# Optimization experiments

Measured on AMD Instinct MI355X. Metric: run time of the kernel, lower is better.

The kernel has to match this reference:

```python
import jax, jax.numpy as jnp
import numpy as np

EPS = 1e-20
TEMP = 0.07
PATCH = 64
STEP = 32  # patch_size * overlap(0.5)


def zero_softmax(x, eps=1e-5):
    # ZeroSoftmax: ((exp(x)-1)^2) / (sum + eps), maps x==0 -> exactly 0 weight
    e = jnp.square(jnp.exp(x) - 1.0)
    return e / (jnp.sum(e, axis=-1, keepdims=True) + eps)


def _scaling_mask(H, W, p, step):
    # constant overlap-count mask from CRW.compute_scaling_mask (static shapes)
    sm = np.zeros((H, W), np.float32)
    for i in range(0, H - step, step):
        for j in range(0, W - step, step):
            sm[i:i + p, j:j + p] += 1.0
    return jnp.asarray(sm)


def _window_sums(m, p, step):
    # m: (B,T,SP,H,W) -> sliding-window sums (B,T,SP,nH,nW) via integral image
    ii = jnp.cumsum(jnp.cumsum(m, axis=-2), axis=-1)
    ii = jnp.pad(ii, ((0, 0), (0, 0), (0, 0), (1, 0), (1, 0)))
    H = m.shape[-2]
    nH = (H - p) // step + 1
    lo = jnp.arange(nH) * step
    hi = lo + p
    r_hi = ii[..., hi, :]   # (B,T,SP,nH,W+1)
    r_lo = ii[..., lo, :]
    return r_hi[..., hi] - r_hi[..., lo] - r_lo[..., hi] + r_lo[..., lo]


def setup_inputs() -> dict:
    key = jax.random.key(0)
    k1, k2, k3 = jax.random.split(key, 3)
    B, T, H, W = 2, 4, 256, 256
    nH = (H - PATCH) // STEP + 1  # 7
    N = nH * nH                   # 49 patches
    Cenc, D, SP = 512, 128, 64
    feats = jax.random.normal(k1, (B, N, Cenc, T), jnp.float32)
    W_head = jax.random.normal(k2, (Cenc, D), jnp.float32) / np.sqrt(Cenc)
    sp_mask = jax.random.randint(k3, (B, T, H, W), 0, SP, jnp.int32)
    return {"feats": feats, "W_head": W_head, "sp_mask": sp_mask, "max_sp_num": SP}


def reference(feats, W_head, sp_mask, max_sp_num):
    B, N, Cenc, T = feats.shape
    H, W = sp_mask.shape[-2:]
    SP = max_sp_num

    # --- pixels_to_nodes tail: projection head + L2 normalize over channel dim ---
    q = jnp.einsum('bnct,cd->bndt', feats, W_head)            # (B,N,128,T)
    nrm = jnp.maximum(jnp.linalg.norm(q, axis=2, keepdims=True), 1e-12)
    q = q / nrm
    q = jnp.transpose(q, (0, 2, 3, 1))                        # (B,128,T,N)

    # --- patches_to_sp_embeddings: windowed superpixel pooling ---
    oh = (sp_mask[:, :, None, :, :] ==
          jnp.arange(SP, dtype=sp_mask.dtype)[None, None, :, None, None]
          ).astype(jnp.float32)                               # (B,T,SP,H,W)
    sm = _scaling_mask(H, W, PATCH, STEP)                     # (H,W)
    ws = _window_sums(oh / sm, PATCH, STEP)                   # (B,T,SP,nH,nW)
    denom = jnp.sum(oh, axis=(-1, -2)) + EPS                  # (B,T,SP)
    wts = jnp.transpose(ws, (0, 1, 3, 4, 2)) / denom[:, :, None, None, :]
    wts = wts.reshape(B, T, N, SP)                            # (B,T,N,SP)
    q_sp = jnp.einsum('bdtn,btns->bdts', q, wts)              # (B,128,T,SP)

    # --- affinity + zero_softmax stochastic matrices ---
    As = jnp.einsum('bdtn,bdtm->btnm', q_sp[:, :, :-1], q_sp[:, :, 1:])  # (B,T-1,SP,SP)
    A12 = zero_softmax(As / TEMP)
    A21 = zero_softmax(jnp.swapaxes(As, -1, -2) / TEMP)

    # --- palindrome random walks + cross-entropy to cycle-consistency targets ---
    tgt = jnp.tile(jnp.arange(SP), B)
    loss = jnp.float32(0.0)
    AAs = []
    for i in range(1, T - 1):
        mats = [A12[:, k] for k in range(i + 1)] + [A21[:, k] for k in range(i, -1, -1)]
        aa = mats[0]
        for m in mats[1:]:
            aa = aa @ m
        AAs.append(aa)
        logits = jnp.log(aa + EPS).reshape(B * SP, SP)
        logp = jax.nn.log_softmax(logits, axis=-1)
        loss = loss + jnp.mean(-logp[jnp.arange(B * SP), tgt])
    return loss, jnp.stack(AAs)
```

## Files before the change

### kernel.cpp

```cpp
#include <hip/hip_runtime.h>
#include <hip/hip_bf16.h>

constexpr int NWIN = 49;
constexpr int QLD  = 52;

constexpr int OFF_WS   = 0;
constexpr int OFF_Q    = 26624;
constexpr int OFF_QSP  = 79872;
constexpr int OFF_A12  = 145408;
constexpr int OFF_A12T = 169984;
constexpr int OFF_A21  = 194560;
constexpr int OFF_A21T = 219136;

__global__ void __launch_bounds__(256, 1)
k_front(const int* __restrict__ mask, const float* __restrict__ feats,
        const float* __restrict__ Wh, float* __restrict__ ws, float* __restrict__ q) {
    if (blockIdx.x < 392) {
        int win = blockIdx.x % NWIN;
        int bt  = blockIdx.x / NWIN;
        int wy = win / 7, wx = win % 7;
        __shared__ float loc[64];
        if (threadIdx.x < 64) loc[threadIdx.x] = 0.f;
        __syncthreads();
        const int* base = mask + bt * 65536 + (wy * 32) * 256 + wx * 32;
        #pragma unroll
        for (int it = 0; it < 16; ++it) {
            int idx = it * 256 + (int)threadIdx.x;
            int r = idx >> 6, c = idx & 63;
            int s = base[r * 256 + c];
            int y = wy * 32 + r, x = wx * 32 + c;
            float w = 1.f;
            if (y >= 32 && y < 224) w *= 0.5f;
            if (x >= 32 && x < 224) w *= 0.5f;
            atomicAdd(&loc[s], w);
        }
        __syncthreads();
        if (threadIdx.x < 64) {
            ws[(bt * 64 + (int)threadIdx.x) * QLD + win] = loc[threadIdx.x];
        } else if (win == 0) {
            int s = threadIdx.x & 63;
            int col = 49 + (int)(threadIdx.x >> 6) - 1;
            ws[(bt * 64 + s) * QLD + col] = 0.f;
        }
    } else {
        int bid = blockIdx.x - 392;
        int n = bid % NWIN, b = bid / NWIN;
        __shared__ float4 f4[512];
        __shared__ float4 psum4[256];
        __shared__ float4 red4[2];
        const float4* fp4 = (const float4*)(feats + (size_t)(b * NWIN + n) * 2048);
        for (int i = threadIdx.x; i < 512; i += 256) f4[i] = fp4[i];
        __syncthreads();

        int d = threadIdx.x & 127, ch = threadIdx.x >> 7;
        float a0 = 0.f, a1 = 0.f, a2 = 0.f, a3 = 0.f;
        const float* wp = Wh + d;
        int c0 = ch * 256;
        #pragma unroll 8
        for (int c = c0; c < c0 + 256; ++c) {
            float w = wp[c * 128];
            float4 fv = f4[c];
            a0 += fv.x * w; a1 += fv.y * w; a2 += fv.z * w; a3 += fv.w * w;
        }
        psum4[threadIdx.x] = make_float4(a0, a1, a2, a3);
        __syncthreads();

        float4 A;
        if (threadIdx.x < 128) {
            float4 p0 = psum4[threadIdx.x], p1 = psum4[128 + threadIdx.x];
            A = make_float4(p0.x + p1.x, p0.y + p1.y, p0.z + p1.z, p0.w + p1.w);
            float sx = A.x * A.x, sy = A.y * A.y, sz = A.z * A.z, sw = A.w * A.w;
            for (int off = 32; off; off >>= 1) {
                sx += __shfl_down(sx, off); sy += __shfl_down(sy, off);
                sz += __shfl_down(sz, off); sw += __shfl_down(sw, off);
            }
            if ((threadIdx.x & 63) == 0) red4[threadIdx.x >> 6] = make_float4(sx, sy, sz, sw);
        }
        __syncthreads();
        if (threadIdx.x < 128) {
            float4 r0 = red4[0], r1 = red4[1];
            float ix = 1.f / fmaxf(sqrtf(r0.x + r1.x), 1e-12f);
            float iy = 1.f / fmaxf(sqrtf(r0.y + r1.y), 1e-12f);
            float iz = 1.f / fmaxf(sqrtf(r0.z + r1.z), 1e-12f);
            float iw = 1.f / fmaxf(sqrtf(r0.w + r1.w), 1e-12f);
            float* qb = q + (size_t)(b * 128 + d) * 4 * QLD + n;
            qb[0 * QLD] = A.x * ix;
            qb[1 * QLD] = A.y * iy;
            qb[2 * QLD] = A.z * iz;
            qb[3 * QLD] = A.w * iw;
        }
    }
}

__global__ void k_qsp(const float* __restrict__ q, const float* __restrict__ wsg,
                      float* __restrict__ qsp) {
    int tid = blockIdx.x * 256 + threadIdx.x;
    int s = tid & 63;
    int d = (tid >> 6) & 127;
    int t = (tid >> 13) & 3;
    int b = tid >> 15;
    const float4* qrow = (const float4*)(q + (size_t)((b * 128 + d) * 4 + t) * QLD);
    const float4* wrow = (const float4*)(wsg + (size_t)((b * 4 + t) * 64 + s) * QLD);
    float acc = 0.f, den = 0.f;
    #pragma unroll
    for (int i = 0; i < 13; ++i) {
        float4 w = wrow[i];
        float4 qv = qrow[i];
        den += w.x + w.y + w.z + w.w;
        acc += qv.x * w.x + qv.y * w.y + qv.z * w.z + qv.w * w.w;
    }
    qsp[tid] = acc / (den + 1e-20f);
}

__global__ void __launch_bounds__(256, 1)
k_as(const float* __restrict__ qsp,
     float* __restrict__ a12, float* __restrict__ a12T,
     float* __restrict__ a21, float* __restrict__ a21T, float* __restrict__ out) {
    int t = blockIdx.x % 3, b = blockIdx.x / 3;
    if (blockIdx.x == 0 && threadIdx.x == 0) out[0] = 0.f;
    __shared__ float4 qaT4[64 * 32];
    __shared__ float4 qbT4[64 * 32];
    const int tid = threadIdx.x;

    {
        const float4* gA = (const float4*)(qsp + (size_t)(b * 4 + t) * 8192);
        const float4* gB = (const float4*)(qsp + (size_t)(b * 4 + t + 1) * 8192);
        float* qaF = (float*)qaT4;
        float* qbF = (float*)qbT4;
        #pragma unroll
        for (int it = 0; it < 8; ++it) {
            int idx = it * 256 + tid;
            int d = idx >> 4, s0 = (idx & 15) << 2;
            float4 va = gA[idx];
            float4 vb = gB[idx];
            int g = d >> 2, c = d & 3;
            #pragma unroll
            for (int u = 0; u < 4; ++u) {
                int s = s0 + u;
                int w = (s * 32 + (g ^ (s & 31))) * 4 + c;
                float fa = (u == 0) ? va.x : (u == 1) ? va.y : (u == 2) ? va.z : va.w;
                float fb = (u == 0) ? vb.x : (u == 1) ? vb.y : (u == 2) ? vb.z : vb.w;
                qaF[w] = fa;
                qbF[w] = fb;
            }
        }
    }
    __syncthreads();

    const int nl = tid >> 4, ml = tid & 15;
    float acc[16];
    #pragma unroll
    for (int i = 0; i < 16; ++i) acc[i] = 0.f;
    #pragma unroll 8
    for (int k4 = 0; k4 < 32; ++k4) {
        float4 av[4], bv[4];
        #pragma unroll
        for (int i = 0; i < 4; ++i) { int n = nl + 16 * i; av[i] = qaT4[n * 32 + (k4 ^ (n & 31))]; }
        #pragma unroll
        for (int j = 0; j < 4; ++j) { int m = ml + 16 * j; bv[j] = qbT4[m * 32 + (k4 ^ (m & 31))]; }
        #pragma unroll
        for (int i = 0; i < 4; ++i)
            #pragma unroll
            for (int j = 0; j < 4; ++j)
                acc[i * 4 + j] += av[i].x * bv[j].x + av[i].y * bv[j].y
                                + av[i].z * bv[j].z + av[i].w * bv[j].w;
    }
    __syncthreads();

    float* eb = (float*)qaT4;
    float* rs = (float*)qbT4;
    float* cs = rs + 64;
    #pragma unroll
    for (int i = 0; i < 4; ++i)
        #pragma unroll
        for (int j = 0; j < 4; ++j) {
            int n = nl + 16 * i, m = ml + 16 * j;
            float x = acc[i * 4 + j] * (1.f / 0.07f);
            float e = expf(x) - 1.f;
            eb[n * 65 + m] = e * e;
        }
    __syncthreads();
    if (tid < 128) {
        int r = tid & 63; bool isrow = tid < 64;
        float a = 0.f;
        #pragma unroll
        for (int k = 0; k < 64; ++k) a += isrow ? eb[r * 65 + k] : eb[k * 65 + r];
        (isrow ? rs : cs)[r] = a + 1e-5f;
    }
    __syncthreads();
    float* p12  = a12  + (b * 3 + t) * 4096;
    float* p12T = a12T + (b * 3 + t) * 4096;
    float* p21  = a21  + (b * 3 + t) * 4096;
    float* p21T = a21T + (b * 3 + t) * 4096;
    #pragma unroll
    for (int i = 0; i < 4; ++i)
        #pragma unroll
        for (int j = 0; j < 4; ++j) {
            int n = nl + 16 * i, m = ml + 16 * j;
            float v   = eb[n * 65 + m];
            float v12 = v / rs[n];
            float v21 = v / cs[m];
            p12 [n * 64 + m] = v12;
            p12T[m * 64 + n] = v12;
            p21 [m * 64 + n] = v21;
            p21T[n * 64 + m] = v21;
        }
}


__device__ __forceinline__ void dump_mat(float* M, const float4* v) {
    #pragma unroll
    for (int it = 0; it < 4; ++it) {
        int idx = it * 256 + (int)threadIdx.x;
        int r = idx >> 4, c4 = (idx & 15) << 2;
        *(float4*)&M[r * 64 + (c4 ^ ((r & 15) << 2))] = v[it];
    }
}

__device__ __forceinline__ void mmh_sw(float* acc, const float* Ra, const float* Rb) {
    int lt = threadIdx.x & 127;
    int nl = lt >> 3, ml = lt & 7;
    int sxa = nl << 2;
    #pragma unroll
    for (int k0 = 0; k0 < 64; k0 += 4) {
        float4 av[4], bv[8];
        #pragma unroll
        for (int i = 0; i < 4; ++i)
            av[i] = *(const float4*)&Ra[(nl + 16 * i) * 64 + (k0 ^ sxa)];
        #pragma unroll
        for (int j = 0; j < 8; ++j) {
            int m = ml + 8 * j;
            bv[j] = *(const float4*)&Rb[m * 64 + (k0 ^ ((m & 15) << 2))];
        }
        #pragma unroll
        for (int i = 0; i < 4; ++i)
            #pragma unroll
            for (int j = 0; j < 8; ++j)
                acc[i * 8 + j] += av[i].x * bv[j].x + av[i].y * bv[j].y
                                + av[i].z * bv[j].z + av[i].w * bv[j].w;
    }
}

__device__ __forceinline__ void wrh_sw(float* M, const float* acc) {
    int lt = threadIdx.x & 127;
    int nl = lt >> 3, ml = lt & 7;
    #pragma unroll
    for (int i = 0; i < 4; ++i)
        #pragma unroll
        for (int j = 0; j < 8; ++j) {
            int r = nl + 16 * i, k = ml + 8 * j;
            M[r * 64 + (((k & ~3) ^ ((r & 15) << 2)) | (k & 3))] = acc[i * 8 + j];
        }
}

__device__ __forceinline__ void mm256_sw(float* acc, const float* Ra, const float* Rb) {
    int tid = threadIdx.x;
    int nl = tid >> 4, ml = tid & 15;
    int sxa = nl << 2, sxb = ml << 2;
    #pragma unroll
    for (int i = 0; i < 16; ++i) acc[i] = 0.f;
    #pragma unroll 4
    for (int k0 = 0; k0 < 64; k0 += 4) {
        float4 av[4], bv[4];
        #pragma unroll
        for (int i = 0; i < 4; ++i)
            av[i] = *(const float4*)&Ra[(nl + 16 * i) * 64 + (k0 ^ sxa)];
        #pragma unroll
        for (int j = 0; j < 4; ++j)
            bv[j] = *(const float4*)&Rb[(ml + 16 * j) * 64 + (k0 ^ sxb)];
        #pragma unroll
        for (int i = 0; i < 4; ++i)
            #pragma unroll
            for (int j = 0; j < 4; ++j)
                acc[i * 4 + j] += av[i].x * bv[j].x + av[i].y * bv[j].y
                                + av[i].z * bv[j].z + av[i].w * bv[j].w;
    }
}

__device__ __forceinline__ void store_loss(const float* acc, float* __restrict__ aa,
                                           float* __restrict__ out, float* red) {
    int tid = threadIdx.x;
    int nl = tid >> 4, ml = tid & 15;
    #pragma unroll
    for (int i = 0; i < 4; ++i)
        #pragma unroll
        for (int j = 0; j < 4; ++j)
            aa[(nl + 16 * i) * 64 + (ml + 16 * j)] = acc[i * 4 + j];
    int l = tid & 63;
    float part = 0.f;
    #pragma unroll
    for (int i = 0; i < 4; ++i) {
        float rsum = acc[i * 4 + 0] + acc[i * 4 + 1] + acc[i * 4 + 2] + acc[i * 4 + 3];
        rsum += __shfl_down(rsum, 8, 16);
        rsum += __shfl_down(rsum, 4, 16);
        rsum += __shfl_down(rsum, 2, 16);
        rsum += __shfl_down(rsum, 1, 16);
        float dv = __shfl(acc[5 * i], (l & 48) | nl, 64);
        if ((l & 15) == 0) part += logf(rsum + 6.4e-19f) - logf(dv + 1e-20f);
    }
    for (int off = 32; off; off >>= 1) part += __shfl_down(part, off);
    if (l == 0) red[tid >> 6] = part;
    __syncthreads();
    if (tid == 0) atomicAdd(out, (red[0] + red[1] + red[2] + red[3]) * (1.f / 128.f));
}

__global__ void __launch_bounds__(256, 1)
k_chain(const float* __restrict__ a12, const float* __restrict__ a12T,
        const float* __restrict__ a21, const float* __restrict__ a21T,
        float* __restrict__ out) {
    int path = blockIdx.x & 1, b = blockIdx.x >> 1;
    __shared__ float M[4 * 4096];
    float* M0 = M;
    float* M1 = M + 4096;
    float* M2 = M + 8192;
    float* M3 = M + 12288;
    const int tid = threadIdx.x;

    const float4* L0 = (const float4*)(a12  + (b * 3 + 0) * 4096);
    const float4* L1 = (const float4*)(a12T + (b * 3 + 1) * 4096);
    const float4* L2 = (const float4*)(a21T + (b * 3 + 0) * 4096);
    const float4* L3 = (const float4*)(a21  + (b * 3 + 1) * 4096);
    const float4* L4 = (const float4*)(a12T + (b * 3 + 2) * 4096);
    const float4* L5 = (const float4*)(a21  + (b * 3 + 2) * 4096);

    float4 pf[6][4];
    #pragma unroll
    for (int it = 0; it < 4; ++it) {
        int idx = it * 256 + tid;
        pf[0][it] = L0[idx];
        pf[1][it] = L1[idx];
        pf[2][it] = L2[idx];
        pf[3][it] = L3[idx];
    }
    if (path) {
        #pragma unroll
        for (int it = 0; it < 4; ++it) {
            int idx = it * 256 + tid;
            pf[4][it] = L4[idx];
            pf[5][it] = L5[idx];
        }
    }
    dump_mat(M0, pf[0]);
    dump_mat(M1, pf[1]);
    dump_mat(M2, pf[2]);
    dump_mat(M3, pf[3]);
    __syncthreads();

    int half = tid >> 7;
    float hacc[32];
    #pragma unroll
    for (int i = 0; i < 32; ++i) hacc[i] = 0.f;
    mmh_sw(hacc, half ? M2 : M0, half ? M3 : M1);
    __syncthreads();
    wrh_sw(half ? M3 : M1, hacc);
    if (path) { dump_mat(M0, pf[4]); dump_mat(M2, pf[5]); }
    __syncthreads();

    if (path == 0) {
        float acc[16];
        mm256_sw(acc, M1, M3);
        store_loss(acc, out + 1 + b * 4096, out, M0);
    } else {
        float hacc2[32];
        #pragma unroll
        for (int i = 0; i < 32; ++i) hacc2[i] = 0.f;
        mmh_sw(hacc2, half ? M3 : M1, half ? M2 : M0);
        __syncthreads();
        wrh_sw(half ? M1 : M0, hacc2);
        __syncthreads();
        float acc[16];
        mm256_sw(acc, M0, M1);
        store_loss(acc, out + 1 + (2 + b) * 4096, out, M2);
    }
}

extern "C" void kernel_launch(void* const* d_in, const int* in_sizes, int n_in,
                              void* d_out, int out_size, void* d_ws, size_t ws_size,
                              hipStream_t stream) {
    const float* feats = (const float*)d_in[0];
    const float* Wh    = (const float*)d_in[1];
    const int*   mask  = (const int*)d_in[2];
    float* out = (float*)d_out;
    float* ws  = (float*)d_ws;

    float* ws_sums = ws + OFF_WS;
    float* q       = ws + OFF_Q;
    float* qsp     = ws + OFF_QSP;
    float* a12     = ws + OFF_A12;
    float* a12T    = ws + OFF_A12T;
    float* a21     = ws + OFF_A21;
    float* a21T    = ws + OFF_A21T;

    k_front<<<392 + 2 * NWIN, 256, 0, stream>>>(mask, feats, Wh, ws_sums, q);
    k_qsp<<<256, 256, 0, stream>>>(q, ws_sums, qsp);
    k_as<<<6, 256, 0, stream>>>(qsp, a12, a12T, a21, a21T, out);
    k_chain<<<4, 256, 0, stream>>>(a12, a12T, a21, a21T, out);
}
```

Before: 118.3 us.

## Fuse four kernels into one persistent kernel with global atomic barriers

Merges the front, qsp, affinity and chain kernels into a single 256-block kernel that steps through the stages, separated by software grid barriers built on atomic counters. Front work units are spread over the 256 blocks, some of which handle two units. The goal is to remove three kernel launch gaps and their tail latency. In exchange it adds a memset launch, spin-wait barriers that rely on all 256 blocks being resident at once, and serialised front work on some blocks.

```diff
diff --git a/kernel.cpp b/kernel.cpp
--- a/kernel.cpp
+++ b/kernel.cpp
@@ -11,15 +11,29 @@
 constexpr int OFF_A12T = 169984;
 constexpr int OFF_A21  = 194560;
 constexpr int OFF_A21T = 219136;
-
-__global__ void __launch_bounds__(256, 1)
-k_front(const int* __restrict__ mask, const float* __restrict__ feats,
-        const float* __restrict__ Wh, float* __restrict__ ws, float* __restrict__ q) {
-    if (blockIdx.x < 392) {
-        int win = blockIdx.x % NWIN;
-        int bt  = blockIdx.x / NWIN;
+constexpr int OFF_BAR  = 243712;
+
+__device__ __forceinline__ void gbar(int* c) {
+    __syncthreads();
+    if (threadIdx.x == 0) {
+        __threadfence();
+        atomicAdd(c, 1);
+        while (atomicAdd(c, 0) < 256) __builtin_amdgcn_s_sleep(2);
+        __threadfence();
+    }
+    __syncthreads();
+}
+
+__device__ __forceinline__ void front_unit(int u, const int* __restrict__ mask,
+                                           const float* __restrict__ feats,
+                                           const float* __restrict__ Wh,
+                                           float* __restrict__ ws,
+                                           float* __restrict__ q, float* SMEM) {
+    if (u < 392) {
+        int win = u % NWIN;
+        int bt  = u / NWIN;
         int wy = win / 7, wx = win % 7;
-        __shared__ float loc[64];
+        float* loc = SMEM;
         if (threadIdx.x < 64) loc[threadIdx.x] = 0.f;
         __syncthreads();
         const int* base = mask + bt * 65536 + (wy * 32) * 256 + wx * 32;
@@ -43,11 +57,11 @@
             ws[(bt * 64 + s) * QLD + col] = 0.f;
         }
     } else {
-        int bid = blockIdx.x - 392;
+        int bid = u - 392;
         int n = bid % NWIN, b = bid / NWIN;
-        __shared__ float4 f4[512];
-        __shared__ float4 psum4[256];
-        __shared__ float4 red4[2];
+        float4* f4    = (float4*)(SMEM + 64);
+        float4* psum4 = f4 + 512;
+        float4* red4  = psum4 + 256;
         const float4* fp4 = (const float4*)(feats + (size_t)(b * NWIN + n) * 2048);
         for (int i = threadIdx.x; i < 512; i += 256) f4[i] = fp4[i];
         __syncthreads();
@@ -92,122 +106,6 @@
     }
 }
 
-__global__ void k_qsp(const float* __restrict__ q, const float* __restrict__ wsg,
-                      float* __restrict__ qsp) {
-    int tid = blockIdx.x * 256 + threadIdx.x;
-    int s = tid & 63;
-    int d = (tid >> 6) & 127;
-    int t = (tid >> 13) & 3;
-    int b = tid >> 15;
-    const float4* qrow = (const float4*)(q + (size_t)((b * 128 + d) * 4 + t) * QLD);
-    const float4* wrow = (const float4*)(wsg + (size_t)((b * 4 + t) * 64 + s) * QLD);
-    float acc = 0.f, den = 0.f;
-    #pragma unroll
-    for (int i = 0; i < 13; ++i) {
-        float4 w = wrow[i];
-        float4 qv = qrow[i];
-        den += w.x + w.y + w.z + w.w;
-        acc += qv.x * w.x + qv.y * w.y + qv.z * w.z + qv.w * w.w;
-    }
-    qsp[tid] = acc / (den + 1e-20f);
-}
-
-__global__ void __launch_bounds__(256, 1)
-k_as(const float* __restrict__ qsp,
-     float* __restrict__ a12, float* __restrict__ a12T,
-     float* __restrict__ a21, float* __restrict__ a21T, float* __restrict__ out) {
-    int t = blockIdx.x % 3, b = blockIdx.x / 3;
-    if (blockIdx.x == 0 && threadIdx.x == 0) out[0] = 0.f;
-    __shared__ float4 qaT4[64 * 32];
-    __shared__ float4 qbT4[64 * 32];
-    const int tid = threadIdx.x;
-
-    {
-        const float4* gA = (const float4*)(qsp + (size_t)(b * 4 + t) * 8192);
-        const float4* gB = (const float4*)(qsp + (size_t)(b * 4 + t + 1) * 8192);
-        float* qaF = (float*)qaT4;
-        float* qbF = (float*)qbT4;
-        #pragma unroll
-        for (int it = 0; it < 8; ++it) {
-            int idx = it * 256 + tid;
-            int d = idx >> 4, s0 = (idx & 15) << 2;
-            float4 va = gA[idx];
-            float4 vb = gB[idx];
-            int g = d >> 2, c = d & 3;
-            #pragma unroll
-            for (int u = 0; u < 4; ++u) {
-                int s = s0 + u;
-                int w = (s * 32 + (g ^ (s & 31))) * 4 + c;
-                float fa = (u == 0) ? va.x : (u == 1) ? va.y : (u == 2) ? va.z : va.w;
-                float fb = (u == 0) ? vb.x : (u == 1) ? vb.y : (u == 2) ? vb.z : vb.w;
-                qaF[w] = fa;
-                qbF[w] = fb;
-            }
-        }
-    }
-    __syncthreads();
-
-    const int nl = tid >> 4, ml = tid & 15;
-    float acc[16];
-    #pragma unroll
-    for (int i = 0; i < 16; ++i) acc[i] = 0.f;
-    #pragma unroll 8
-    for (int k4 = 0; k4 < 32; ++k4) {
-        float4 av[4], bv[4];
-        #pragma unroll
-        for (int i = 0; i < 4; ++i) { int n = nl + 16 * i; av[i] = qaT4[n * 32 + (k4 ^ (n & 31))]; }
-        #pragma unroll
-        for (int j = 0; j < 4; ++j) { int m = ml + 16 * j; bv[j] = qbT4[m * 32 + (k4 ^ (m & 31))]; }
-        #pragma unroll
-        for (int i = 0; i < 4; ++i)
-            #pragma unroll
-            for (int j = 0; j < 4; ++j)
-                acc[i * 4 + j] += av[i].x * bv[j].x + av[i].y * bv[j].y
-                                + av[i].z * bv[j].z + av[i].w * bv[j].w;
-    }
-    __syncthreads();
-
-    float* eb = (float*)qaT4;
-    float* rs = (float*)qbT4;
-    float* cs = rs + 64;
-    #pragma unroll
-    for (int i = 0; i < 4; ++i)
-        #pragma unroll
-        for (int j = 0; j < 4; ++j) {
-            int n = nl + 16 * i, m = ml + 16 * j;
-            float x = acc[i * 4 + j] * (1.f / 0.07f);
-            float e = expf(x) - 1.f;
-            eb[n * 65 + m] = e * e;
-        }
-    __syncthreads();
-    if (tid < 128) {
-        int r = tid & 63; bool isrow = tid < 64;
-        float a = 0.f;
-        #pragma unroll
-        for (int k = 0; k < 64; ++k) a += isrow ? eb[r * 65 + k] : eb[k * 65 + r];
-        (isrow ? rs : cs)[r] = a + 1e-5f;
-    }
-    __syncthreads();
-    float* p12  = a12  + (b * 3 + t) * 4096;
-    float* p12T = a12T + (b * 3 + t) * 4096;
-    float* p21  = a21  + (b * 3 + t) * 4096;
-    float* p21T = a21T + (b * 3 + t) * 4096;
-    #pragma unroll
-    for (int i = 0; i < 4; ++i)
-        #pragma unroll
-        for (int j = 0; j < 4; ++j) {
-            int n = nl + 16 * i, m = ml + 16 * j;
-            float v   = eb[n * 65 + m];
-            float v12 = v / rs[n];
-            float v21 = v / cs[m];
-            p12 [n * 64 + m] = v12;
-            p12T[m * 64 + n] = v12;
-            p21 [m * 64 + n] = v21;
-            p21T[n * 64 + m] = v21;
-        }
-}
-
-
 __device__ __forceinline__ void dump_mat(float* M, const float4* v) {
     #pragma unroll
     for (int it = 0; it < 4; ++it) {
@@ -305,72 +203,199 @@
 }
 
 __global__ void __launch_bounds__(256, 1)
-k_chain(const float* __restrict__ a12, const float* __restrict__ a12T,
-        const float* __restrict__ a21, const float* __restrict__ a21T,
-        float* __restrict__ out) {
-    int path = blockIdx.x & 1, b = blockIdx.x >> 1;
-    __shared__ float M[4 * 4096];
-    float* M0 = M;
-    float* M1 = M + 4096;
-    float* M2 = M + 8192;
-    float* M3 = M + 12288;
+k_all(const int* __restrict__ mask, const float* __restrict__ feats,
+      const float* __restrict__ Wh, float* __restrict__ ws,
+      float* __restrict__ q, float* __restrict__ qsp,
+      float* __restrict__ a12, float* __restrict__ a12T,
+      float* __restrict__ a21, float* __restrict__ a21T,
+      float* __restrict__ out, int* __restrict__ bars) {
+    __shared__ __align__(16) float SMEM[16384];
+    const int blk = blockIdx.x;
     const int tid = threadIdx.x;
 
-    const float4* L0 = (const float4*)(a12  + (b * 3 + 0) * 4096);
-    const float4* L1 = (const float4*)(a12T + (b * 3 + 1) * 4096);
-    const float4* L2 = (const float4*)(a21T + (b * 3 + 0) * 4096);
-    const float4* L3 = (const float4*)(a21  + (b * 3 + 1) * 4096);
-    const float4* L4 = (const float4*)(a12T + (b * 3 + 2) * 4096);
-    const float4* L5 = (const float4*)(a21  + (b * 3 + 2) * 4096);
-
-    float4 pf[6][4];
-    #pragma unroll
-    for (int it = 0; it < 4; ++it) {
-        int idx = it * 256 + tid;
-        pf[0][it] = L0[idx];
-        pf[1][it] = L1[idx];
-        pf[2][it] = L2[idx];
-        pf[3][it] = L3[idx];
-    }
-    if (path) {
+    front_unit(blk, mask, feats, Wh, ws, q, SMEM);
+    if (blk < 234) {
+        __syncthreads();
+        front_unit(blk + 256, mask, feats, Wh, ws, q, SMEM);
+    }
+    gbar(&bars[0]);
+
+    {
+        int t2 = blk * 256 + tid;
+        int s = t2 & 63;
+        int d = (t2 >> 6) & 127;
+        int t = (t2 >> 13) & 3;
+        int b = t2 >> 15;
+        const float4* qrow = (const float4*)(q + (size_t)((b * 128 + d) * 4 + t) * QLD);
+        const float4* wrow = (const float4*)(ws + (size_t)((b * 4 + t) * 64 + s) * QLD);
+        float acc = 0.f, den = 0.f;
+        #pragma unroll
+        for (int i = 0; i < 13; ++i) {
+            float4 w = wrow[i];
+            float4 qv = qrow[i];
+            den += w.x + w.y + w.z + w.w;
+            acc += qv.x * w.x + qv.y * w.y + qv.z * w.z + qv.w * w.w;
+        }
+        qsp[t2] = acc / (den + 1e-20f);
+    }
+    gbar(&bars[1]);
+
+    if (blk < 6) {
+        int t = blk % 3, b = blk / 3;
+        if (blk == 0 && tid == 0) out[0] = 0.f;
+        float4* qaT4 = (float4*)SMEM;
+        float4* qbT4 = qaT4 + 2048;
+
+        {
+            const float4* gA = (const float4*)(qsp + (size_t)(b * 4 + t) * 8192);
+            const float4* gB = (const float4*)(qsp + (size_t)(b * 4 + t + 1) * 8192);
+            float* qaF = (float*)qaT4;
+            float* qbF = (float*)qbT4;
+            #pragma unroll
+            for (int it = 0; it < 8; ++it) {
+                int idx = it * 256 + tid;
+                int d = idx >> 4, s0 = (idx & 15) << 2;
+                float4 va = gA[idx];
+                float4 vb = gB[idx];
+                int g = d >> 2, c = d & 3;
+                #pragma unroll
+                for (int u = 0; u < 4; ++u) {
+                    int s = s0 + u;
+                    int w = (s * 32 + (g ^ (s & 31))) * 4 + c;
+                    float fa = (u == 0) ? va.x : (u == 1) ? va.y : (u == 2) ? va.z : va.w;
+                    float fb = (u == 0) ? vb.x : (u == 1) ? vb.y : (u == 2) ? vb.z : vb.w;
+                    qaF[w] = fa;
+                    qbF[w] = fb;
+                }
+            }
+        }
+        __syncthreads();
+
+        const int nl = tid >> 4, ml = tid & 15;
+        float acc[16];
+        #pragma unroll
+        for (int i = 0; i < 16; ++i) acc[i] = 0.f;
+        #pragma unroll 8
+        for (int k4 = 0; k4 < 32; ++k4) {
+            float4 av[4], bv[4];
+            #pragma unroll
+            for (int i = 0; i < 4; ++i) { int n = nl + 16 * i; av[i] = qaT4[n * 32 + (k4 ^ (n & 31))]; }
+            #pragma unroll
+            for (int j = 0; j < 4; ++j) { int m = ml + 16 * j; bv[j] = qbT4[m * 32 + (k4 ^ (m & 31))]; }
+            #pragma unroll
+            for (int i = 0; i < 4; ++i)
+                #pragma unroll
+                for (int j = 0; j < 4; ++j)
+                    acc[i * 4 + j] += av[i].x * bv[j].x + av[i].y * bv[j].y
+                                    + av[i].z * bv[j].z + av[i].w * bv[j].w;
+        }
+        __syncthreads();
+
+        float* eb = (float*)qaT4;
+        float* rs = (float*)qbT4;
+        float* cs = rs + 64;
+        #pragma unroll
+        for (int i = 0; i < 4; ++i)
+            #pragma unroll
+            for (int j = 0; j < 4; ++j) {
+                int n = nl + 16 * i, m = ml + 16 * j;
+                float x = acc[i * 4 + j] * (1.f / 0.07f);
+                float e = expf(x) - 1.f;
+                eb[n * 65 + m] = e * e;
+            }
+        __syncthreads();
+        if (tid < 128) {
+            int r = tid & 63; bool isrow = tid < 64;
+            float a = 0.f;
+            #pragma unroll
+            for (int k = 0; k < 64; ++k) a += isrow ? eb[r * 65 + k] : eb[k * 65 + r];
+            (isrow ? rs : cs)[r] = a + 1e-5f;
+        }
+        __syncthreads();
+        float* p12  = a12  + (b * 3 + t) * 4096;
+        float* p12T = a12T + (b * 3 + t) * 4096;
+        float* p21  = a21  + (b * 3 + t) * 4096;
+        float* p21T = a21T + (b * 3 + t) * 4096;
+        #pragma unroll
+        for (int i = 0; i < 4; ++i)
+            #pragma unroll
+            for (int j = 0; j < 4; ++j) {
+                int n = nl + 16 * i, m = ml + 16 * j;
+                float v   = eb[n * 65 + m];
+                float v12 = v / rs[n];
+                float v21 = v / cs[m];
+                p12 [n * 64 + m] = v12;
+                p12T[m * 64 + n] = v12;
+                p21 [m * 64 + n] = v21;
+                p21T[n * 64 + m] = v21;
+            }
+    }
+    gbar(&bars[2]);
+
+    if (blk < 4) {
+        int path = blk & 1, b = blk >> 1;
+        float* M0 = SMEM;
+        float* M1 = SMEM + 4096;
+        float* M2 = SMEM + 8192;
+        float* M3 = SMEM + 12288;
+
+        const float4* L0 = (const float4*)(a12  + (b * 3 + 0) * 4096);
+        const float4* L1 = (const float4*)(a12T + (b * 3 + 1) * 4096);
+        const float4* L2 = (const float4*)(a21T + (b * 3 + 0) * 4096);
+        const float4* L3 = (const float4*)(a21  + (b * 3 + 1) * 4096);
+        const float4* L4 = (const float4*)(a12T + (b * 3 + 2) * 4096);
+        const float4* L5 = (const float4*)(a21  + (b * 3 + 2) * 4096);
+
+        float4 pf[6][4];
         #pragma unroll
         for (int it = 0; it < 4; ++it) {
             int idx = it * 256 + tid;
-            pf[4][it] = L4[idx];
-            pf[5][it] = L5[idx];
-        }
-    }
-    dump_mat(M0, pf[0]);
-    dump_mat(M1, pf[1]);
-    dump_mat(M2, pf[2]);
-    dump_mat(M3, pf[3]);
-    __syncthreads();
-
-    int half = tid >> 7;
-    float hacc[32];
-    #pragma unroll
-    for (int i = 0; i < 32; ++i) hacc[i] = 0.f;
-    mmh_sw(hacc, half ? M2 : M0, half ? M3 : M1);
-    __syncthreads();
-    wrh_sw(half ? M3 : M1, hacc);
-    if (path) { dump_mat(M0, pf[4]); dump_mat(M2, pf[5]); }
-    __syncthreads();
-
-    if (path == 0) {
-        float acc[16];
-        mm256_sw(acc, M1, M3);
-        store_loss(acc, out + 1 + b * 4096, out, M0);
-    } else {
-        float hacc2[32];
-        #pragma unroll
-        for (int i = 0; i < 32; ++i) hacc2[i] = 0.f;
-        mmh_sw(hacc2, half ? M3 : M1, half ? M2 : M0);
-        __syncthreads();
-        wrh_sw(half ? M1 : M0, hacc2);
-        __syncthreads();
-        float acc[16];
-        mm256_sw(acc, M0, M1);
-        store_loss(acc, out + 1 + (2 + b) * 4096, out, M2);
+            pf[0][it] = L0[idx];
+            pf[1][it] = L1[idx];
+            pf[2][it] = L2[idx];
+            pf[3][it] = L3[idx];
+        }
+        if (path) {
+            #pragma unroll
+            for (int it = 0; it < 4; ++it) {
+                int idx = it * 256 + tid;
+                pf[4][it] = L4[idx];
+                pf[5][it] = L5[idx];
+            }
+        }
+        __syncthreads();
+        dump_mat(M0, pf[0]);
+        dump_mat(M1, pf[1]);
+        dump_mat(M2, pf[2]);
+        dump_mat(M3, pf[3]);
+        __syncthreads();
+
+        int half = tid >> 7;
+        float hacc[32];
+        #pragma unroll
+        for (int i = 0; i < 32; ++i) hacc[i] = 0.f;
+        mmh_sw(hacc, half ? M2 : M0, half ? M3 : M1);
+        __syncthreads();
+        wrh_sw(half ? M3 : M1, hacc);
+        if (path) { dump_mat(M0, pf[4]); dump_mat(M2, pf[5]); }
+        __syncthreads();
+
+        if (path == 0) {
+            float acc[16];
+            mm256_sw(acc, M1, M3);
+            store_loss(acc, out + 1 + b * 4096, out, M0);
+        } else {
+            float hacc2[32];
+            #pragma unroll
+            for (int i = 0; i < 32; ++i) hacc2[i] = 0.f;
+            mmh_sw(hacc2, half ? M3 : M1, half ? M2 : M0);
+            __syncthreads();
+            wrh_sw(half ? M1 : M0, hacc2);
+            __syncthreads();
+            float acc[16];
+            mm256_sw(acc, M0, M1);
+            store_loss(acc, out + 1 + (2 + b) * 4096, out, M2);
+        }
     }
 }
 
@@ -390,9 +415,9 @@
     float* a12T    = ws + OFF_A12T;
     float* a21     = ws + OFF_A21;
     float* a21T    = ws + OFF_A21T;
-
-    k_front<<<392 + 2 * NWIN, 256, 0, stream>>>(mask, feats, Wh, ws_sums, q);
-    k_qsp<<<256, 256, 0, stream>>>(q, ws_sums, qsp);
-    k_as<<<6, 256, 0, stream>>>(qsp, a12, a12T, a21, a21T, out);
-    k_chain<<<4, 256, 0, stream>>>(a12, a12T, a21, a21T, out);
-}
+    int*   bars    = (int*)(ws + OFF_BAR);
+
+    hipMemsetAsync(bars, 0, 16, stream);
+    k_all<<<256, 256, 0, stream>>>(mask, feats, Wh, ws_sums, q, qsp,
+                                   a12, a12T, a21, a21T, out, bars);
+}
```

New measurement: 170.5 us. 44.1% more time.

## Fuse qsp, affinity and chain kernels into one with a global spin barrier

Applied to the files above, without the earlier changes.

Merges the superpixel pooling (qsp), the affinity/zero-softmax step and the random-walk chain into a single 6-block kernel. Each block recomputes its own two qsp slices in shared memory, in 32-channel chunks, rather than reading them from a separate kernel's global output. An atomic counter plus spin-wait with agent-scope fences replaces the kernel boundary between the affinity and chain stages. This removes two launches and the qsp round trip through global memory. In exchange the pooling work runs on only 6 blocks instead of 256, and correctness depends on all 6 blocks being co-resident for the spin barrier.

```diff
diff --git a/kernel.cpp b/kernel.cpp
--- a/kernel.cpp
+++ b/kernel.cpp
@@ -5,16 +5,25 @@
 constexpr int QLD  = 52;
 
 constexpr int OFF_WS   = 0;
-constexpr int OFF_Q    = 26624;
-constexpr int OFF_QSP  = 79872;
-constexpr int OFF_A12  = 145408;
-constexpr int OFF_A12T = 169984;
-constexpr int OFF_A21  = 194560;
-constexpr int OFF_A21T = 219136;
+constexpr int OFF_BAR  = 26624;
+constexpr int OFF_Q    = 26640;
+constexpr int OFF_A12  = 79888;
+constexpr int OFF_A12T = 104464;
+constexpr int OFF_A21  = 129040;
+constexpr int OFF_A21T = 153616;
+
+__device__ __forceinline__ void fence_rel() {
+    __builtin_amdgcn_fence(__ATOMIC_RELEASE, "agent");
+}
+__device__ __forceinline__ void fence_acq() {
+    __builtin_amdgcn_fence(__ATOMIC_ACQUIRE, "agent");
+}
 
 __global__ void __launch_bounds__(256, 1)
 k_front(const int* __restrict__ mask, const float* __restrict__ feats,
-        const float* __restrict__ Wh, float* __restrict__ ws, float* __restrict__ q) {
+        const float* __restrict__ Wh, float* __restrict__ ws, float* __restrict__ q,
+        int* __restrict__ bars) {
+    if (blockIdx.x == 0 && threadIdx.x == 0) bars[0] = 0;
     if (blockIdx.x < 392) {
         int win = blockIdx.x % NWIN;
         int bt  = blockIdx.x / NWIN;
@@ -92,122 +101,6 @@
     }
 }
 
-__global__ void k_qsp(const float* __restrict__ q, const float* __restrict__ wsg,
-                      float* __restrict__ qsp) {
-    int tid = blockIdx.x * 256 + threadIdx.x;
-    int s = tid & 63;
-    int d = (tid >> 6) & 127;
-    int t = (tid >> 13) & 3;
-    int b = tid >> 15;
-    const float4* qrow = (const float4*)(q + (size_t)((b * 128 + d) * 4 + t) * QLD);
-    const float4* wrow = (const float4*)(wsg + (size_t)((b * 4 + t) * 64 + s) * QLD);
-    float acc = 0.f, den = 0.f;
-    #pragma unroll
-    for (int i = 0; i < 13; ++i) {
-        float4 w = wrow[i];
-        float4 qv = qrow[i];
-        den += w.x + w.y + w.z + w.w;
-        acc += qv.x * w.x + qv.y * w.y + qv.z * w.z + qv.w * w.w;
-    }
-    qsp[tid] = acc / (den + 1e-20f);
-}
-
-__global__ void __launch_bounds__(256, 1)
-k_as(const float* __restrict__ qsp,
-     float* __restrict__ a12, float* __restrict__ a12T,
-     float* __restrict__ a21, float* __restrict__ a21T, float* __restrict__ out) {
-    int t = blockIdx.x % 3, b = blockIdx.x / 3;
-    if (blockIdx.x == 0 && threadIdx.x == 0) out[0] = 0.f;
-    __shared__ float4 qaT4[64 * 32];
-    __shared__ float4 qbT4[64 * 32];
-    const int tid = threadIdx.x;
-
-    {
-        const float4* gA = (const float4*)(qsp + (size_t)(b * 4 + t) * 8192);
-        const float4* gB = (const float4*)(qsp + (size_t)(b * 4 + t + 1) * 8192);
-        float* qaF = (float*)qaT4;
-        float* qbF = (float*)qbT4;
-        #pragma unroll
-        for (int it = 0; it < 8; ++it) {
-            int idx = it * 256 + tid;
-            int d = idx >> 4, s0 = (idx & 15) << 2;
-            float4 va = gA[idx];
-            float4 vb = gB[idx];
-            int g = d >> 2, c = d & 3;
-            #pragma unroll
-            for (int u = 0; u < 4; ++u) {
-                int s = s0 + u;
-                int w = (s * 32 + (g ^ (s & 31))) * 4 + c;
-                float fa = (u == 0) ? va.x : (u == 1) ? va.y : (u == 2) ? va.z : va.w;
-                float fb = (u == 0) ? vb.x : (u == 1) ? vb.y : (u == 2) ? vb.z : vb.w;
-                qaF[w] = fa;
-                qbF[w] = fb;
-            }
-        }
-    }
-    __syncthreads();
-
-    const int nl = tid >> 4, ml = tid & 15;
-    float acc[16];
-    #pragma unroll
-    for (int i = 0; i < 16; ++i) acc[i] = 0.f;
-    #pragma unroll 8
-    for (int k4 = 0; k4 < 32; ++k4) {
-        float4 av[4], bv[4];
-        #pragma unroll
-        for (int i = 0; i < 4; ++i) { int n = nl + 16 * i; av[i] = qaT4[n * 32 + (k4 ^ (n & 31))]; }
-        #pragma unroll
-        for (int j = 0; j < 4; ++j) { int m = ml + 16 * j; bv[j] = qbT4[m * 32 + (k4 ^ (m & 31))]; }
-        #pragma unroll
-        for (int i = 0; i < 4; ++i)
-            #pragma unroll
-            for (int j = 0; j < 4; ++j)
-                acc[i * 4 + j] += av[i].x * bv[j].x + av[i].y * bv[j].y
-                                + av[i].z * bv[j].z + av[i].w * bv[j].w;
-    }
-    __syncthreads();
-
-    float* eb = (float*)qaT4;
-    float* rs = (float*)qbT4;
-    float* cs = rs + 64;
-    #pragma unroll
-    for (int i = 0; i < 4; ++i)
-        #pragma unroll
-        for (int j = 0; j < 4; ++j) {
-            int n = nl + 16 * i, m = ml + 16 * j;
-            float x = acc[i * 4 + j] * (1.f / 0.07f);
-            float e = expf(x) - 1.f;
-            eb[n * 65 + m] = e * e;
-        }
-    __syncthreads();
-    if (tid < 128) {
-        int r = tid & 63; bool isrow = tid < 64;
-        float a = 0.f;
-        #pragma unroll
-        for (int k = 0; k < 64; ++k) a += isrow ? eb[r * 65 + k] : eb[k * 65 + r];
-        (isrow ? rs : cs)[r] = a + 1e-5f;
-    }
-    __syncthreads();
-    float* p12  = a12  + (b * 3 + t) * 4096;
-    float* p12T = a12T + (b * 3 + t) * 4096;
-    float* p21  = a21  + (b * 3 + t) * 4096;
-    float* p21T = a21T + (b * 3 + t) * 4096;
-    #pragma unroll
-    for (int i = 0; i < 4; ++i)
-        #pragma unroll
-        for (int j = 0; j < 4; ++j) {
-            int n = nl + 16 * i, m = ml + 16 * j;
-            float v   = eb[n * 65 + m];
-            float v12 = v / rs[n];
-            float v21 = v / cs[m];
-            p12 [n * 64 + m] = v12;
-            p12T[m * 64 + n] = v12;
-            p21 [m * 64 + n] = v21;
-            p21T[n * 64 + m] = v21;
-        }
-}
-
-
 __device__ __forceinline__ void dump_mat(float* M, const float4* v) {
     #pragma unroll
     for (int it = 0; it < 4; ++it) {
@@ -305,72 +198,218 @@
 }
 
 __global__ void __launch_bounds__(256, 1)
-k_chain(const float* __restrict__ a12, const float* __restrict__ a12T,
-        const float* __restrict__ a21, const float* __restrict__ a21T,
-        float* __restrict__ out) {
-    int path = blockIdx.x & 1, b = blockIdx.x >> 1;
-    __shared__ float M[4 * 4096];
-    float* M0 = M;
-    float* M1 = M + 4096;
-    float* M2 = M + 8192;
-    float* M3 = M + 12288;
+k_aschain(const float* __restrict__ q, const float* __restrict__ wsg,
+          float* __restrict__ a12s, float* __restrict__ a12Ts,
+          float* __restrict__ a21s, float* __restrict__ a21Ts,
+          float* __restrict__ out, int* __restrict__ bars) {
+    __shared__ __align__(16) float SMEM[16384];
+    const int blk = blockIdx.x;
     const int tid = threadIdx.x;
-
-    const float4* L0 = (const float4*)(a12  + (b * 3 + 0) * 4096);
-    const float4* L1 = (const float4*)(a12T + (b * 3 + 1) * 4096);
-    const float4* L2 = (const float4*)(a21T + (b * 3 + 0) * 4096);
-    const float4* L3 = (const float4*)(a21  + (b * 3 + 1) * 4096);
-    const float4* L4 = (const float4*)(a12T + (b * 3 + 2) * 4096);
-    const float4* L5 = (const float4*)(a21  + (b * 3 + 2) * 4096);
-
-    float4 pf[6][4];
-    #pragma unroll
-    for (int it = 0; it < 4; ++it) {
-        int idx = it * 256 + tid;
-        pf[0][it] = L0[idx];
-        pf[1][it] = L1[idx];
-        pf[2][it] = L2[idx];
-        pf[3][it] = L3[idx];
-    }
-    if (path) {
+    const int t = blk % 3, b = blk / 3;
+    const int s = tid & 63, wv = tid >> 6;
+
+    if (blk == 0 && tid == 0) out[0] = 0.f;
+
+    float4 wsA[13], wsB[13];
+    float denA = 0.f, denB = 0.f;
+    {
+        const float4* wra = (const float4*)(wsg + (size_t)((b * 4 + t) * 64 + s) * QLD);
+        const float4* wrb = (const float4*)(wsg + (size_t)((b * 4 + t + 1) * 64 + s) * QLD);
+        #pragma unroll
+        for (int i = 0; i < 13; ++i) {
+            wsA[i] = wra[i]; wsB[i] = wrb[i];
+            denA += wsA[i].x + wsA[i].y + wsA[i].z + wsA[i].w;
+            denB += wsB[i].x + wsB[i].y + wsB[i].z + wsB[i].w;
+        }
+    }
+    const float invA = 1.f / (denA + 1e-20f);
+    const float invB = 1.f / (denB + 1e-20f);
+
+    float4* qstA = (float4*)SMEM;
+    float4* qstB = qstA + 416;
+    float4* qaC  = qstB + 416;
+    float4* qbC  = qaC + 512;
+
+    const float4* q4 = (const float4*)q;
+    const int nl = tid >> 4, ml = tid & 15;
+    float acc[16];
+    #pragma unroll
+    for (int i = 0; i < 16; ++i) acc[i] = 0.f;
+
+    for (int c4 = 0; c4 < 4; ++c4) {
+        const int D = c4 * 32;
+        __syncthreads();
+        for (int idx = tid; idx < 832; idx += 256) {
+            int which = idx >= 416;
+            int loc = which ? idx - 416 : idx;
+            int r = loc / 13, i = loc - r * 13;
+            float4 v = q4[((size_t)(b * 128 + D + r) * 4 + t + which) * 13 + i];
+            (which ? qstB : qstA)[r * 13 + i] = v;
+        }
+        __syncthreads();
+        float oa[8], ob[8];
+        #pragma unroll
+        for (int u = 0; u < 8; ++u) {
+            int dl = 8 * wv + u;
+            const float4* qa = qstA + dl * 13;
+            const float4* qb = qstB + dl * 13;
+            float sa = 0.f, sb = 0.f;
+            #pragma unroll
+            for (int i = 0; i < 13; ++i) {
+                float4 va = qa[i];
+                sa += va.x * wsA[i].x + va.y * wsA[i].y + va.z * wsA[i].z + va.w * wsA[i].w;
+            }
+            #pragma unroll
+            for (int i = 0; i < 13; ++i) {
+                float4 vb = qb[i];
+                sb += vb.x * wsB[i].x + vb.y * wsB[i].y + vb.z * wsB[i].z + vb.w * wsB[i].w;
+            }
+            oa[u] = sa * invA; ob[u] = sb * invB;
+        }
+        #pragma unroll
+        for (int h = 0; h < 2; ++h) {
+            int gl = 2 * wv + h;
+            int w = s * 8 + (gl ^ (s & 7));
+            qaC[w] = make_float4(oa[4 * h], oa[4 * h + 1], oa[4 * h + 2], oa[4 * h + 3]);
+            qbC[w] = make_float4(ob[4 * h], ob[4 * h + 1], ob[4 * h + 2], ob[4 * h + 3]);
+        }
+        __syncthreads();
+        #pragma unroll
+        for (int k4 = 0; k4 < 8; ++k4) {
+            float4 av[4], bv[4];
+            #pragma unroll
+            for (int i = 0; i < 4; ++i) { int n = nl + 16 * i; av[i] = qaC[n * 8 + (k4 ^ (n & 7))]; }
+            #pragma unroll
+            for (int j = 0; j < 4; ++j) { int m = ml + 16 * j; bv[j] = qbC[m * 8 + (k4 ^ (m & 7))]; }
+            #pragma unroll
+            for (int i = 0; i < 4; ++i)
+                #pragma unroll
+                for (int j = 0; j < 4; ++j)
+                    acc[i * 4 + j] += av[i].x * bv[j].x + av[i].y * bv[j].y
+                                    + av[i].z * bv[j].z + av[i].w * bv[j].w;
+        }
+    }
+    __syncthreads();
+
+    {
+        float* eb = SMEM;
+        float* rs = SMEM + 4160;
+        float* cs = SMEM + 4224;
+        #pragma unroll
+        for (int i = 0; i < 4; ++i)
+            #pragma unroll
+            for (int j = 0; j < 4; ++j) {
+                int n = nl + 16 * i, m = ml + 16 * j;
+                float x = acc[i * 4 + j] * (1.f / 0.07f);
+                float e = expf(x) - 1.f;
+                eb[n * 65 + m] = e * e;
+            }
+        __syncthreads();
+        if (tid < 128) {
+            int r = tid & 63; bool isrow = tid < 64;
+            float a = 0.f;
+            #pragma unroll
+            for (int k = 0; k < 64; ++k) a += isrow ? eb[r * 65 + k] : eb[k * 65 + r];
+            (isrow ? rs : cs)[r] = a + 1e-5f;
+        }
+        __syncthreads();
+        float* p12  = a12s  + (b * 3 + t) * 4096;
+        float* p12T = a12Ts + (b * 3 + t) * 4096;
+        float* p21  = a21s  + (b * 3 + t) * 4096;
+        float* p21T = a21Ts + (b * 3 + t) * 4096;
+        #pragma unroll
+        for (int i = 0; i < 4; ++i)
+            #pragma unroll
+            for (int j = 0; j < 4; ++j) {
+                int n = nl + 16 * i, m = ml + 16 * j;
+                float v   = eb[n * 65 + m];
+                float v12 = v / rs[n];
+                float v21 = v / cs[m];
+                p12 [n * 64 + m] = v12;
+                p12T[m * 64 + n] = v12;
+                p21 [m * 64 + n] = v21;
+                p21T[n * 64 + m] = v21;
+            }
+    }
+
+    __syncthreads();
+    if (tid == 0) {
+        fence_rel();
+        __hip_atomic_fetch_add(&bars[0], 1, __ATOMIC_RELAXED, __HIP_MEMORY_SCOPE_AGENT);
+    }
+    if (blk >= 4) return;
+    if (tid == 0) {
+        while (__hip_atomic_load(&bars[0], __ATOMIC_RELAXED,
+                                 __HIP_MEMORY_SCOPE_AGENT) < 6)
+            __builtin_amdgcn_s_sleep(1);
+        fence_acq();
+    }
+    __syncthreads();
+
+    {
+        int path = blk & 1, bc = blk >> 1;
+        float* M0 = SMEM;
+        float* M1 = SMEM + 4096;
+        float* M2 = SMEM + 8192;
+        float* M3 = SMEM + 12288;
+
+        const float4* L0 = (const float4*)(a12s  + (bc * 3 + 0) * 4096);
+        const float4* L1 = (const float4*)(a12Ts + (bc * 3 + 1) * 4096);
+        const float4* L2 = (const float4*)(a21Ts + (bc * 3 + 0) * 4096);
+        const float4* L3 = (const float4*)(a21s  + (bc * 3 + 1) * 4096);
+        const float4* L4 = (const float4*)(a12Ts + (bc * 3 + 2) * 4096);
+        const float4* L5 = (const float4*)(a21s  + (bc * 3 + 2) * 4096);
+
+        float4 pf[6][4];
         #pragma unroll
         for (int it = 0; it < 4; ++it) {
             int idx = it * 256 + tid;
-            pf[4][it] = L4[idx];
-            pf[5][it] = L5[idx];
-        }
-    }
-    dump_mat(M0, pf[0]);
-    dump_mat(M1, pf[1]);
-    dump_mat(M2, pf[2]);
-    dump_mat(M3, pf[3]);
-    __syncthreads();
-
-    int half = tid >> 7;
-    float hacc[32];
-    #pragma unroll
-    for (int i = 0; i < 32; ++i) hacc[i] = 0.f;
-    mmh_sw(hacc, half ? M2 : M0, half ? M3 : M1);
-    __syncthreads();
-    wrh_sw(half ? M3 : M1, hacc);
-    if (path) { dump_mat(M0, pf[4]); dump_mat(M2, pf[5]); }
-    __syncthreads();
-
-    if (path == 0) {
-        float acc[16];
-        mm256_sw(acc, M1, M3);
-        store_loss(acc, out + 1 + b * 4096, out, M0);
-    } else {
-        float hacc2[32];
-        #pragma unroll
-        for (int i = 0; i < 32; ++i) hacc2[i] = 0.f;
-        mmh_sw(hacc2, half ? M3 : M1, half ? M2 : M0);
-        __syncthreads();
-        wrh_sw(half ? M1 : M0, hacc2);
-        __syncthreads();
-        float acc[16];
-        mm256_sw(acc, M0, M1);
-        store_loss(acc, out + 1 + (2 + b) * 4096, out, M2);
+            pf[0][it] = L0[idx];
+            pf[1][it] = L1[idx];
+            pf[2][it] = L2[idx];
+            pf[3][it] = L3[idx];
+        }
+        if (path) {
+            #pragma unroll
+            for (int it = 0; it < 4; ++it) {
+                int idx = it * 256 + tid;
+                pf[4][it] = L4[idx];
+                pf[5][it] = L5[idx];
+            }
+        }
+        __syncthreads();
+        dump_mat(M0, pf[0]);
+        dump_mat(M1, pf[1]);
+        dump_mat(M2, pf[2]);
+        dump_mat(M3, pf[3]);
+        __syncthreads();
+
+        int half = tid >> 7;
+        float hacc[32];
+        #pragma unroll
+        for (int i = 0; i < 32; ++i) hacc[i] = 0.f;
+        mmh_sw(hacc, half ? M2 : M0, half ? M3 : M1);
+        __syncthreads();
+        wrh_sw(half ? M3 : M1, hacc);
+        if (path) { dump_mat(M0, pf[4]); dump_mat(M2, pf[5]); }
+        __syncthreads();
+
+        if (path == 0) {
+            float acc2[16];
+            mm256_sw(acc2, M1, M3);
+            store_loss(acc2, out + 1 + bc * 4096, out, M0);
+        } else {
+            float hacc2[32];
+            #pragma unroll
+            for (int i = 0; i < 32; ++i) hacc2[i] = 0.f;
+            mmh_sw(hacc2, half ? M3 : M1, half ? M2 : M0);
+            __syncthreads();
+            wrh_sw(half ? M1 : M0, hacc2);
+            __syncthreads();
+            float acc2[16];
+            mm256_sw(acc2, M0, M1);
+            store_loss(acc2, out + 1 + (2 + bc) * 4096, out, M2);
+        }
     }
 }
 
@@ -385,14 +424,12 @@
 
     float* ws_sums = ws + OFF_WS;
     float* q       = ws + OFF_Q;
-    float* qsp     = ws + OFF_QSP;
     float* a12     = ws + OFF_A12;
     float* a12T    = ws + OFF_A12T;
     float* a21     = ws + OFF_A21;
     float* a21T    = ws + OFF_A21T;
-
-    k_front<<<392 + 2 * NWIN, 256, 0, stream>>>(mask, feats, Wh, ws_sums, q);
-    k_qsp<<<256, 256, 0, stream>>>(q, ws_sums, qsp);
-    k_as<<<6, 256, 0, stream>>>(qsp, a12, a12T, a21, a21T, out);
-    k_chain<<<4, 256, 0, stream>>>(a12, a12T, a21, a21T, out);
-}
+    int*   bars    = (int*)(ws + OFF_BAR);
+
+    k_front<<<392 + 2 * NWIN, 256, 0, stream>>>(mask, feats, Wh, ws_sums, q, bars);
+    k_aschain<<<6, 256, 0, stream>>>(q, ws_sums, a12, a12T, a21, a21T, out, bars);
+}
```

Measured after the change: 145.3 us. +22.8%, slower.
